# Kernel optimization log

Hardware: AMD Instinct MI355X
Metric: run time of the kernel (lower is better)

The kernel has to match this reference:

```python
import jax, jax.numpy as jnp
import numpy as np
from jax import lax

NSAMPLE = 16
NEG_SLOPE = 0.1


def leaky(x):
    return jnp.where(x >= 0, x, NEG_SLOPE * x)


def setup_inputs() -> dict:
    key = jax.random.key(0)
    ks = jax.random.split(key, 8)
    B, N1, N2, D = 4, 4096, 4096, 64
    C_in, C_mid, C_out = D + D + 3, 128, 128  # 131 -> 128 -> 128
    xyz1 = jax.random.normal(ks[0], (B, 3, N1), jnp.float32)
    xyz2 = jax.random.normal(ks[1], (B, 3, N2), jnp.float32)
    points1 = jax.random.normal(ks[2], (B, D, N1), jnp.float32)
    points2 = jax.random.normal(ks[3], (B, D, N2), jnp.float32)
    W1 = jax.random.normal(ks[4], (C_mid, C_in), jnp.float32) * 0.05
    b1 = jnp.zeros((C_mid,), jnp.float32)
    W2 = jax.random.normal(ks[5], (C_out, C_mid), jnp.float32) * 0.05
    b2 = jnp.zeros((C_out,), jnp.float32)
    return {"xyz1": xyz1, "xyz2": xyz2, "points1": points1, "points2": points2,
            "W1": W1, "b1": b1, "W2": W2, "b2": b2}


def reference(xyz1, xyz2, points1, points2, W1, b1, W2, b2):
    B, _, N1 = xyz1.shape
    x1 = jnp.transpose(xyz1, (0, 2, 1))      # [B,N1,3]
    x2 = jnp.transpose(xyz2, (0, 2, 1))      # [B,N2,3]
    p1 = jnp.transpose(points1, (0, 2, 1))   # [B,N1,D1]
    p2 = jnp.transpose(points2, (0, 2, 1))   # [B,N2,D2]

    # knn_point: k smallest squared distances from each x1 point into x2
    d2 = (jnp.sum(x1 * x1, -1)[:, :, None]
          + jnp.sum(x2 * x2, -1)[:, None, :]
          - 2.0 * jnp.einsum('bnc,bmc->bnm', x1, x2))  # [B,N1,N2]
    _, knn_idx = lax.top_k(-d2, NSAMPLE)     # [B,N1,K]

    bidx = jnp.arange(B)[:, None, None]
    neighbor_xyz = x2[bidx, knn_idx]         # [B,N1,K,3]
    direction_xyz = neighbor_xyz - x1[:, :, None, :]
    gp2 = p2[bidx, knn_idx]                  # [B,N1,K,D2]
    gp1 = jnp.broadcast_to(p1[:, :, None, :], (B, N1, NSAMPLE, p1.shape[-1]))
    feat = jnp.concatenate([gp1, gp2, direction_xyz], axis=-1)  # [B,N1,K,131]

    h = leaky(jnp.einsum('oc,bnkc->bnko', W1, feat) + b1)
    h = leaky(jnp.einsum('oc,bnkc->bnko', W2, h) + b2)           # [B,N1,K,C_out]

    dist = jnp.maximum(jnp.linalg.norm(direction_xyz, axis=3), 1e-10)  # [B,N1,K]
    inv = 1.0 / dist
    weights = inv / jnp.sum(inv, axis=2, keepdims=True)          # [B,N1,K]

    cost = jnp.einsum('bnk,bnko->bon', weights, h)               # [B,C_out,N1]
    return cost
```

## Files before the change

kernel.cpp:

```cpp
#include <hip/hip_runtime.h>

typedef unsigned short u16;
typedef unsigned int u32;
typedef unsigned long long u64;
typedef __bf16 bf16x8 __attribute__((ext_vector_type(8)));
typedef float f32x4 __attribute__((ext_vector_type(4)));

#define MFMA16(a, b, c) __builtin_amdgcn_mfma_f32_16x16x32_bf16(a, b, c, 0, 0, 0)

static __device__ __forceinline__ u16 f2bf(float f) {
  union { float f; u32 u; } v; v.f = f;
  u32 u = v.u;
  u32 r = (u + 0x7FFFu + ((u >> 16) & 1u)) >> 16;
  return (u16)r;
}

static __device__ __forceinline__ bf16x8 ld16(const u16* p) {
  return __builtin_bit_cast(bf16x8, *(const uint4*)p);
}

static __device__ __forceinline__ u64 u64min(u64 a, u64 b) { return a < b ? a : b; }

static __device__ __forceinline__ u64 bitonic64(u64 v, int lane) {
#pragma unroll
  for (int k = 2; k <= 64; k <<= 1) {
#pragma unroll
    for (int j = k >> 1; j > 0; j >>= 1) {
      u64 o = __shfl_xor(v, j, 64);
      bool up = ((lane & k) == 0);
      bool lower = ((lane & j) == 0);
      u64 mn = v < o ? v : o;
      u64 mx = v < o ? o : v;
      v = (lower == up) ? mn : mx;
    }
  }
  return v;
}

static __device__ __forceinline__ float bitonic64f(float v, int lane) {
#pragma unroll
  for (int k = 2; k <= 64; k <<= 1) {
#pragma unroll
    for (int j = k >> 1; j > 0; j >>= 1) {
      float o = __shfl_xor(v, j, 64);
      bool up = ((lane & k) == 0);
      bool lower = ((lane & j) == 0);
      float mn = fminf(v, o);
      float mx = fmaxf(v, o);
      v = (lower == up) ? mn : mx;
    }
  }
  return v;
}

static __device__ __forceinline__ u32 fkey(float f) {
  u32 bb = __float_as_uint(f);
  u32 sgn = (u32)((int)bb >> 31);
  return bb ^ (sgn | 0x80000000u);
}

static __device__ __forceinline__ float d2of(float x, float y, float z, float s1,
                                             f32x4 c) {
  float dt = __builtin_fmaf(z, c[2], __builtin_fmaf(y, c[1], __fmul_rn(x, c[0])));
  return __fsub_rn(__fadd_rn(s1, c[3]), __fmul_rn(2.0f, dt));
}

__global__ __launch_bounds__(256) void transpose_cast(const float* __restrict__ src,
                                                      u16* __restrict__ dst) {
  __shared__ __align__(4) u16 tile[64 * 66];
  const int t = threadIdx.x;
  const int b = blockIdx.x >> 6;
  const int n0 = (blockIdx.x & 63) << 6;
  const float* sp = src + ((size_t)b << 18);
#pragma unroll
  for (int i = 0; i < 16; i++) {
    int d = (i << 2) + (t >> 6);
    int n = t & 63;
    tile[n * 66 + d] = f2bf(sp[((size_t)d << 12) + n0 + n]);
  }
  __syncthreads();
  u16* dp = dst + ((size_t)(b * 4096 + n0) << 6);
#pragma unroll
  for (int i = 0; i < 8; i++) {
    int n = (i << 3) + (t >> 5);
    int dp2 = t & 31;
    *(u32*)(dp + n * 64 + (dp2 << 1)) = *(const u32*)(tile + n * 66 + (dp2 << 1));
  }
}

__global__ __launch_bounds__(256) void prep_w(const float* __restrict__ W1,
                                              const float* __restrict__ W2,
                                              u16* __restrict__ W1b,
                                              u16* __restrict__ W2b) {
  int t = blockIdx.x * 256 + threadIdx.x;
  if (t < 128 * 160) {
    int r = t / 160, c = t - r * 160;
    W1b[t] = (c < 131) ? f2bf(W1[r * 131 + c]) : (u16)0;
  } else {
    int u = t - 128 * 160;
    W2b[u] = f2bf(W2[u]);
  }
}

__global__ __launch_bounds__(256, 2) void knn_kernel(const float* __restrict__ xyz1,
                                                     const float* __restrict__ xyz2,
                                                     int* __restrict__ knn) {
  __shared__ __align__(16) float candL[4096 * 4];
  __shared__ u64 surv[4][64];
  __shared__ u32 cnt[4];
  const int t = threadIdx.x;
  const int lane = t & 63;
  const int w = t >> 6;
  const int b = blockIdx.x >> 7;
  const int rbase = (blockIdx.x & 127) << 5;
  const float* X1 = xyz1 + b * 12288;
  const float* X2 = xyz2 + b * 12288;

#pragma unroll
  for (int j2 = 0; j2 < 16; j2++) {
    int m = j2 * 256 + t;
    float x = X2[m], y = X2[4096 + m], z = X2[8192 + m];
    float s2 = __fadd_rn(__fadd_rn(__fmul_rn(x, x), __fmul_rn(y, y)),
                         __fmul_rn(z, z));
    f32x4 pk = {x, y, z, s2};
    *(f32x4*)&candL[m * 4] = pk;
  }
  __syncthreads();

#pragma unroll 1
  for (int r = 0; r < 8; r++) {
    const int n = rbase + (w << 3) + r;
    const int row = b * 4096 + n;
    const float x = X1[n], y = X1[4096 + n], z = X1[8192 + n];
    const float s1 = __fadd_rn(__fadd_rn(__fmul_rn(x, x), __fmul_rn(y, y)),
                               __fmul_rn(z, z));

    float keys[64];
    float fm = 3e38f;
#pragma unroll
    for (int j = 0; j < 64; j++) {
      const int m = (j << 6) + lane;
      f32x4 c = *(const f32x4*)&candL[m * 4];
      float d = d2of(x, y, z, s1, c);
      keys[j] = d;
      fm = fminf(fm, d);
    }

    float tauf = __shfl(bitonic64f(fm, lane), 15, 64);

    if (lane == 0) cnt[w] = 0;
#pragma unroll
    for (int j = 0; j < 64; j++) {
      if (keys[j] <= tauf) {
        u64 k64 = ((u64)fkey(keys[j]) << 32) | (u32)((j << 6) + lane);
        u32 slot = atomicAdd(&cnt[w], 1u);
        if (slot < 64) surv[w][slot] = k64;
      }
    }
    u32 S = cnt[w];

    if (S <= 64) {
      u64 v = (lane < (int)S) ? surv[w][lane] : ~0ull;
      v = bitonic64(v, lane);
      if (lane < 16) knn[row * 16 + lane] = (int)(v & 0xFFFFFFFFull);
    } else {
      u64 prev = 0;
      for (int rr = 0; rr < 16; rr++) {
        u64 lm = ~0ull;
#pragma unroll
        for (int j = 0; j < 64; j++) {
          u64 k64 = ((u64)fkey(keys[j]) << 32) | (u32)((j << 6) + lane);
          if (k64 > prev && k64 < lm) lm = k64;
        }
        u64 gm = lm;
#pragma unroll
        for (int off = 32; off; off >>= 1) gm = u64min(gm, __shfl_xor(gm, off, 64));
        if (lane == 0) knn[row * 16 + rr] = (int)(gm & 0xFFFFFFFFull);
        prev = gm;
      }
    }
  }
}

__global__ __launch_bounds__(256, 3) void mlp_kernel(
    const float* __restrict__ xyz1, const float* __restrict__ xyz2,
    const u16* __restrict__ p1t, const u16* __restrict__ p2t,
    const int* __restrict__ knn,
    const u16* __restrict__ W1b, const float* __restrict__ b1,
    const u16* __restrict__ W2b, const float* __restrict__ b2,
    float* __restrict__ out) {
  __shared__ __align__(16) u16 F[128 * 168];
  __shared__ __align__(16) float winv[128];
  __shared__ __align__(16) float wnorm[128];
  __shared__ __align__(16) float outbuf[128 * 12];
  const int t = threadIdx.x;
  const int g = blockIdx.x;
  const int b = g >> 9;
  const int rbase = (g & 511) << 3;

  {
    const int m = t >> 1, half = t & 1;
    const int n1 = rbase + (m >> 4);
    const uint4* s1p = (const uint4*)(p1t + ((size_t)(b * 4096 + n1) << 6)) + half * 4;
    uint4* d1p = (uint4*)(F + m * 168) + half * 4;
    d1p[0] = s1p[0]; d1p[1] = s1p[1]; d1p[2] = s1p[2]; d1p[3] = s1p[3];
    const int idx = knn[(((size_t)(b * 4096 + n1)) << 4) + (m & 15)];
    const uint4* s2p = (const uint4*)(p2t + ((size_t)(b * 4096 + idx) << 6)) + half * 4;
    uint4* d2p = (uint4*)(F + m * 168 + 64) + half * 4;
    d2p[0] = s2p[0]; d2p[1] = s2p[1]; d2p[2] = s2p[2]; d2p[3] = s2p[3];
  }
  if (t < 128) {
    const int m = t;
    const int n1 = rbase + (m >> 4);
    const int idx = knn[(((size_t)(b * 4096 + n1)) << 4) + (m & 15)];
    const float* X1 = xyz1 + b * 12288;
    const float* X2 = xyz2 + b * 12288;
    float dx = X2[idx] - X1[n1];
    float dy = X2[4096 + idx] - X1[4096 + n1];
    float dz = X2[8192 + idx] - X1[8192 + n1];
    u32 u0 = (u32)f2bf(dx) | ((u32)f2bf(dy) << 16);
    u32 u1 = (u32)f2bf(dz);
    uint4 pk = make_uint4(u0, u1, 0u, 0u);
    *(uint4*)(F + m * 168 + 128) = pk;
    float d = sqrtf(dx * dx + dy * dy + dz * dz);
    winv[m] = 1.0f / fmaxf(d, 1e-10f);
  } else {
    const int m = t - 128;
    uint4 zz = make_uint4(0u, 0u, 0u, 0u);
    uint4* zp = (uint4*)(F + m * 168 + 136);
    zp[0] = zz; zp[1] = zz; zp[2] = zz; zp[3] = zz;
  }
  __syncthreads();

  if (t < 128) {
    const int r = t >> 4;
    float s = 0.f;
#pragma unroll
    for (int k = 0; k < 16; k++) s += winv[(r << 4) + k];
    wnorm[t] = winv[t] / s;
  }

  const int lane = t & 63;
  const int wid = t >> 6;
  const int l15 = lane & 15;
  const int quad = lane >> 4;
  const int koff = quad << 3;
  const int nbase = wid << 5;

  f32x4 acc[8][2];
  const f32x4 z4 = {0.f, 0.f, 0.f, 0.f};
#pragma unroll
  for (int i = 0; i < 8; i++)
#pragma unroll
    for (int j = 0; j < 2; j++) acc[i][j] = z4;

#pragma unroll
  for (int s = 0; s < 5; s++) {
    bf16x8 bf0 = ld16(W1b + (nbase + l15) * 160 + s * 32 + koff);
    bf16x8 bf1 = ld16(W1b + (nbase + 16 + l15) * 160 + s * 32 + koff);
#pragma unroll
    for (int mt = 0; mt < 8; mt++) {
      bf16x8 a = ld16(F + (mt * 16 + l15) * 168 + s * 32 + koff);
      acc[mt][0] = MFMA16(a, bf0, acc[mt][0]);
      acc[mt][1] = MFMA16(a, bf1, acc[mt][1]);
    }
  }
  __syncthreads();

  {
    const float bv0 = b1[nbase + l15];
    const float bv1 = b1[nbase + 16 + l15];
#pragma unroll
    for (int mt = 0; mt < 8; mt++) {
      u16* hrow = F + (mt * 16 + quad * 4) * 168;
#pragma unroll
      for (int r = 0; r < 4; r++) {
        float zv0 = acc[mt][0][r] + bv0;
        zv0 = (zv0 >= 0.f) ? zv0 : 0.1f * zv0;
        hrow[r * 168 + nbase + l15] = f2bf(zv0);
        float zv1 = acc[mt][1][r] + bv1;
        zv1 = (zv1 >= 0.f) ? zv1 : 0.1f * zv1;
        hrow[r * 168 + nbase + 16 + l15] = f2bf(zv1);
      }
    }
  }
  __syncthreads();

  f32x4 acc2[8][2];
#pragma unroll
  for (int i = 0; i < 8; i++)
#pragma unroll
    for (int j = 0; j < 2; j++) acc2[i][j] = z4;

#pragma unroll
  for (int s = 0; s < 4; s++) {
    bf16x8 bf0 = ld16(W2b + (nbase + l15) * 128 + s * 32 + koff);
    bf16x8 bf1 = ld16(W2b + (nbase + 16 + l15) * 128 + s * 32 + koff);
#pragma unroll
    for (int mt = 0; mt < 8; mt++) {
      bf16x8 a = ld16(F + (mt * 16 + l15) * 168 + s * 32 + koff);
      acc2[mt][0] = MFMA16(a, bf0, acc2[mt][0]);
      acc2[mt][1] = MFMA16(a, bf1, acc2[mt][1]);
    }
  }

  {
    const float bv0 = b2[nbase + l15];
    const float bv1 = b2[nbase + 16 + l15];
#pragma unroll
    for (int mt = 0; mt < 8; mt++) {
      const f32x4 w4 = *(const f32x4*)&wnorm[(mt << 4) + (quad << 2)];
      float p0 = 0.f, p1 = 0.f;
#pragma unroll
      for (int r = 0; r < 4; r++) {
        float zv0 = acc2[mt][0][r] + bv0;
        zv0 = (zv0 >= 0.f) ? zv0 : 0.1f * zv0;
        p0 += zv0 * w4[r];
        float zv1 = acc2[mt][1][r] + bv1;
        zv1 = (zv1 >= 0.f) ? zv1 : 0.1f * zv1;
        p1 += zv1 * w4[r];
      }
      p0 += __shfl_xor(p0, 16); p0 += __shfl_xor(p0, 32);
      p1 += __shfl_xor(p1, 16); p1 += __shfl_xor(p1, 32);
      if (quad == 0) {
        outbuf[(nbase + l15) * 12 + mt] = p0;
        outbuf[(nbase + 16 + l15) * 12 + mt] = p1;
      }
    }
  }
  __syncthreads();
  {
    const int ch = t >> 1, half = t & 1;
    f32x4 v = *(const f32x4*)&outbuf[ch * 12 + (half << 2)];
    float* op = out + (((size_t)(b * 128 + ch)) << 12) + rbase + (half << 2);
    *(f32x4*)op = v;
  }
}

extern "C" void kernel_launch(void* const* d_in, const int* in_sizes, int n_in,
                              void* d_out, int out_size, void* d_ws, size_t ws_size,
                              hipStream_t stream) {
  const float* xyz1 = (const float*)d_in[0];
  const float* xyz2 = (const float*)d_in[1];
  const float* points1 = (const float*)d_in[2];
  const float* points2 = (const float*)d_in[3];
  const float* W1 = (const float*)d_in[4];
  const float* b1 = (const float*)d_in[5];
  const float* W2 = (const float*)d_in[6];
  const float* b2 = (const float*)d_in[7];
  float* out = (float*)d_out;

  char* ws = (char*)d_ws;
  int* knn = (int*)ws;
  u16* p1t = (u16*)(ws + 1048576);
  u16* p2t = (u16*)(ws + 3145728);
  u16* W1b = (u16*)(ws + 5242880);
  u16* W2b = (u16*)(ws + 5283840);

  hipLaunchKernelGGL(transpose_cast, dim3(256), dim3(256), 0, stream, points1, p1t);
  hipLaunchKernelGGL(transpose_cast, dim3(256), dim3(256), 0, stream, points2, p2t);
  hipLaunchKernelGGL(prep_w, dim3(144), dim3(256), 0, stream, W1, W2, W1b, W2b);
  hipLaunchKernelGGL(knn_kernel, dim3(512), dim3(256), 0, stream, xyz1, xyz2, knn);
  hipLaunchKernelGGL(mlp_kernel, dim3(2048), dim3(256), 0, stream,
                     xyz1, xyz2, p1t, p2t, knn, W1b, b1, W2b, b2, out);
}
```

Baseline: 165.7 us.

## Fuse prep kernels and precompute packed xyz2 candidates, halve knn LDS

Merges the two transpose_cast launches and prep_w into one prep_fused launch, which also precomputes packed (x,y,z,|x|^2) candidates for xyz2 into a global buffer. knn_kernel now loads only half of the candidates into shared memory (32 KB instead of 64 KB) and reads the other half straight from global memory/cache. The aim is fewer launches, no repeated per-block norm computation, and lower LDS use so more knn blocks can be resident per CU. The risk is that the global reads in the inner distance loop have higher latency than LDS.

New measurement: 236.5 us. 42.7% more time.

```diff
diff --git a/kernel.cpp b/kernel.cpp
--- a/kernel.cpp
+++ b/kernel.cpp
@@ -65,47 +65,62 @@
   return __fsub_rn(__fadd_rn(s1, c[3]), __fmul_rn(2.0f, dt));
 }
 
-__global__ __launch_bounds__(256) void transpose_cast(const float* __restrict__ src,
-                                                      u16* __restrict__ dst) {
+__global__ __launch_bounds__(256) void prep_fused(
+    const float* __restrict__ points1, const float* __restrict__ points2,
+    const float* __restrict__ W1, const float* __restrict__ W2,
+    const float* __restrict__ xyz2,
+    u16* __restrict__ p1t, u16* __restrict__ p2t,
+    u16* __restrict__ W1b, u16* __restrict__ W2b,
+    f32x4* __restrict__ candG) {
   __shared__ __align__(4) u16 tile[64 * 66];
+  const int g = blockIdx.x;
   const int t = threadIdx.x;
-  const int b = blockIdx.x >> 6;
-  const int n0 = (blockIdx.x & 63) << 6;
-  const float* sp = src + ((size_t)b << 18);
-#pragma unroll
-  for (int i = 0; i < 16; i++) {
-    int d = (i << 2) + (t >> 6);
-    int n = t & 63;
-    tile[n * 66 + d] = f2bf(sp[((size_t)d << 12) + n0 + n]);
-  }
-  __syncthreads();
-  u16* dp = dst + ((size_t)(b * 4096 + n0) << 6);
-#pragma unroll
-  for (int i = 0; i < 8; i++) {
-    int n = (i << 3) + (t >> 5);
-    int dp2 = t & 31;
-    *(u32*)(dp + n * 64 + (dp2 << 1)) = *(const u32*)(tile + n * 66 + (dp2 << 1));
-  }
-}
-
-__global__ __launch_bounds__(256) void prep_w(const float* __restrict__ W1,
-                                              const float* __restrict__ W2,
-                                              u16* __restrict__ W1b,
-                                              u16* __restrict__ W2b) {
-  int t = blockIdx.x * 256 + threadIdx.x;
-  if (t < 128 * 160) {
-    int r = t / 160, c = t - r * 160;
-    W1b[t] = (c < 131) ? f2bf(W1[r * 131 + c]) : (u16)0;
+  if (g < 512) {
+    const float* src = (g < 256) ? points1 : points2;
+    u16* dst = (g < 256) ? p1t : p2t;
+    const int gb = g & 255;
+    const int b = gb >> 6;
+    const int n0 = (gb & 63) << 6;
+    const float* sp = src + ((size_t)b << 18);
+#pragma unroll
+    for (int i = 0; i < 16; i++) {
+      int d = (i << 2) + (t >> 6);
+      int n = t & 63;
+      tile[n * 66 + d] = f2bf(sp[((size_t)d << 12) + n0 + n]);
+    }
+    __syncthreads();
+    u16* dp = dst + ((size_t)(b * 4096 + n0) << 6);
+#pragma unroll
+    for (int i = 0; i < 8; i++) {
+      int n = (i << 3) + (t >> 5);
+      int dp2 = t & 31;
+      *(u32*)(dp + n * 64 + (dp2 << 1)) = *(const u32*)(tile + n * 66 + (dp2 << 1));
+    }
+  } else if (g < 656) {
+    int i = (g - 512) * 256 + t;
+    if (i < 128 * 160) {
+      int r = i / 160, c = i - r * 160;
+      W1b[i] = (c < 131) ? f2bf(W1[r * 131 + c]) : (u16)0;
+    } else {
+      int u = i - 128 * 160;
+      W2b[u] = f2bf(W2[u]);
+    }
   } else {
-    int u = t - 128 * 160;
-    W2b[u] = f2bf(W2[u]);
+    int i = (g - 656) * 256 + t;
+    int b = i >> 12, m = i & 4095;
+    const float* X2 = xyz2 + b * 12288;
+    float x = X2[m], y = X2[4096 + m], z = X2[8192 + m];
+    float s2 = __fadd_rn(__fadd_rn(__fmul_rn(x, x), __fmul_rn(y, y)),
+                         __fmul_rn(z, z));
+    f32x4 pk = {x, y, z, s2};
+    candG[i] = pk;
   }
 }
 
 __global__ __launch_bounds__(256, 2) void knn_kernel(const float* __restrict__ xyz1,
-                                                     const float* __restrict__ xyz2,
+                                                     const f32x4* __restrict__ candG,
                                                      int* __restrict__ knn) {
-  __shared__ __align__(16) float candL[4096 * 4];
+  __shared__ __align__(16) f32x4 candL[2048];
   __shared__ u64 surv[4][64];
   __shared__ u32 cnt[4];
   const int t = threadIdx.x;
@@ -114,16 +129,12 @@
   const int b = blockIdx.x >> 7;
   const int rbase = (blockIdx.x & 127) << 5;
   const float* X1 = xyz1 + b * 12288;
-  const float* X2 = xyz2 + b * 12288;
-
-#pragma unroll
-  for (int j2 = 0; j2 < 16; j2++) {
-    int m = j2 * 256 + t;
-    float x = X2[m], y = X2[4096 + m], z = X2[8192 + m];
-    float s2 = __fadd_rn(__fadd_rn(__fmul_rn(x, x), __fmul_rn(y, y)),
-                         __fmul_rn(z, z));
-    f32x4 pk = {x, y, z, s2};
-    *(f32x4*)&candL[m * 4] = pk;
+  const f32x4* CG = candG + b * 4096;
+
+#pragma unroll
+  for (int i = 0; i < 8; i++) {
+    int m = i * 256 + t;
+    candL[m] = CG[m];
   }
   __syncthreads();
 
@@ -140,7 +151,7 @@
 #pragma unroll
     for (int j = 0; j < 64; j++) {
       const int m = (j << 6) + lane;
-      f32x4 c = *(const f32x4*)&candL[m * 4];
+      f32x4 c = (j < 32) ? candL[m] : CG[m];
       float d = d2of(x, y, z, s1, c);
       keys[j] = d;
       fm = fminf(fm, d);
@@ -356,11 +367,11 @@
   u16* p2t = (u16*)(ws + 3145728);
   u16* W1b = (u16*)(ws + 5242880);
   u16* W2b = (u16*)(ws + 5283840);
-
-  hipLaunchKernelGGL(transpose_cast, dim3(256), dim3(256), 0, stream, points1, p1t);
-  hipLaunchKernelGGL(transpose_cast, dim3(256), dim3(256), 0, stream, points2, p2t);
-  hipLaunchKernelGGL(prep_w, dim3(144), dim3(256), 0, stream, W1, W2, W1b, W2b);
-  hipLaunchKernelGGL(knn_kernel, dim3(512), dim3(256), 0, stream, xyz1, xyz2, knn);
+  f32x4* candG = (f32x4*)(ws + 5316608);
+
+  hipLaunchKernelGGL(prep_fused, dim3(720), dim3(256), 0, stream,
+                     points1, points2, W1, W2, xyz2, p1t, p2t, W1b, W2b, candG);
+  hipLaunchKernelGGL(knn_kernel, dim3(512), dim3(256), 0, stream, xyz1, candG, knn);
   hipLaunchKernelGGL(mlp_kernel, dim3(2048), dim3(256), 0, stream,
                      xyz1, xyz2, p1t, p2t, knn, W1b, b1, W2b, b2, out);
 }
```
